# Kernel tuning notes

Measured on AMD Instinct MI355X. Metric: run time of the kernel, lower is better.

The kernel has to match this reference:

```python
import jax, jax.numpy as jnp
import numpy as np

DIM = 384
HEADS = 8
SR = 2
BN_EPS = 1e-5


def setup_inputs() -> dict:
    key = jax.random.key(0)
    ks = jax.random.split(key, 8)
    B, Hh, Ww = 4, 64, 64
    N = Hh * Ww
    Nk = (Hh // SR) * (Ww // SR)
    w = lambda k, s: jax.random.normal(k, s, jnp.float32) * 0.02
    return {
        "x": jax.random.normal(ks[0], (B, N, DIM), jnp.float32),
        "relative_pos": jax.random.normal(ks[1], (HEADS, N, Nk), jnp.float32) * 0.02,
        "H": Hh,
        "W": Ww,
        "Wq": w(ks[2], (DIM, DIM)),
        "Wk": w(ks[3], (DIM, DIM)),
        "Wv": w(ks[4], (DIM, DIM)),
        "Wp": w(ks[5], (DIM, DIM)),
        "bp": jnp.zeros((DIM,), jnp.float32),
        "sr_w": w(ks[6], (DIM, 1, SR, SR)),  # depthwise conv, OIHW with groups=DIM
        "sr_b": jnp.zeros((DIM,), jnp.float32),
        "bn_gamma": jnp.ones((DIM,), jnp.float32),
        "bn_beta": jnp.zeros((DIM,), jnp.float32),
        "bn_mean": jnp.zeros((DIM,), jnp.float32),
        "bn_var": jnp.ones((DIM,), jnp.float32),
    }


def reference(x, relative_pos, Wq, Wk, Wv, Wp, bp, sr_w, sr_b,
              bn_gamma, bn_beta, bn_mean, bn_var, H, W):
    B, N, C = x.shape
    hd = C // HEADS
    scale = hd ** (-0.5)
    # q projection -> [B, heads, N, hd]
    q = (x @ Wq.T).reshape(B, N, HEADS, hd).transpose(0, 2, 1, 3)
    # spatial reduction: depthwise conv stride SR + BatchNorm (eval mode)
    x_ = x.transpose(0, 2, 1).reshape(B, C, H, W)
    y = jax.lax.conv_general_dilated(
        x_, sr_w, window_strides=(SR, SR), padding="VALID",
        feature_group_count=C,
        dimension_numbers=("NCHW", "OIHW", "NCHW"))
    y = y + sr_b[None, :, None, None]
    inv = jax.lax.rsqrt(bn_var + BN_EPS) * bn_gamma
    y = (y - bn_mean[None, :, None, None]) * inv[None, :, None, None] \
        + bn_beta[None, :, None, None]
    xk = y.reshape(B, C, -1).transpose(0, 2, 1)  # [B, Nk, C]
    Nk = xk.shape[1]
    k = (xk @ Wk.T).reshape(B, Nk, HEADS, hd).transpose(0, 2, 1, 3)
    v = (xk @ Wv.T).reshape(B, Nk, HEADS, hd).transpose(0, 2, 1, 3)
    # scores with additive relative-position bias (broadcast over batch)
    attn = jnp.einsum("bhnd,bhmd->bhnm", q, k) * scale + relative_pos
    attn = jax.nn.softmax(attn, axis=-1)
    out = jnp.einsum("bhnm,bhmd->bhnd", attn, v)
    out = out.transpose(0, 2, 1, 3).reshape(B, N, C)
    return out @ Wp.T + bp
```

## Files before the change

### kernel.cpp

```cpp
#include <hip/hip_runtime.h>
#include <hip/hip_bf16.h>

#define LOG2E 1.4426950408889634f

typedef short bf16x8 __attribute__((ext_vector_type(8)));
typedef float f32x4  __attribute__((ext_vector_type(4)));

#define OFF_BPf  16
#define OFF_SRWf (OFF_BPf + 384)
#define OFF_SRBf (OFF_SRWf + 1536)
#define OFF_GAf  (OFF_SRBf + 384)
#define OFF_BEf  (OFF_GAf + 384)
#define OFF_MUf  (OFF_BEf + 384)
#define OFF_VAf  (OFF_MUf + 384)
#define U_XB 7712
#define U_WQ (U_XB + 6291456)
#define U_WK (U_WQ + 147456)
#define U_WV (U_WK + 147456)
#define U_WP (U_WV + 147456)
#define U_XK (U_WP + 147456)
#define U_QB (U_XK + 1572864)
#define U_KB (U_QB + 6291456)
#define U_VT (U_KB + 1572864)
#define U_OB (U_VT + 1572864)

static __device__ __forceinline__ float bfu(unsigned short u){ return __uint_as_float(((unsigned)u) << 16); }
static __device__ __forceinline__ float bf_lo(unsigned v){ return __uint_as_float(v << 16); }
static __device__ __forceinline__ float bf_hi(unsigned v){ return __uint_as_float(v & 0xFFFF0000u); }
static __device__ __forceinline__ unsigned short f2bf(float f){
  unsigned u = __float_as_uint(f);
  u += 0x7FFFu + ((u >> 16) & 1u);
  return (unsigned short)(u >> 16);
}
static __device__ __forceinline__ unsigned pk2bf(float a, float b){
  return (unsigned)f2bf(a) | ((unsigned)f2bf(b) << 16);
}

__global__ void detect_bf16(const unsigned* __restrict__ xraw, int* __restrict__ flag){
  unsigned w = xraw[threadIdx.x];
  unsigned e = (w >> 7) & 0xFFu;
  unsigned long long m = __ballot(e >= 118u && e <= 137u);
  if (threadIdx.x == 0) *flag = (__popcll(m) >= 40) ? 1 : 0;
}

static __device__ __forceinline__ void cp8_bf(unsigned short* dst, const void* src, int off, bool bf){
  if (bf) { *(uint4*)dst = *(const uint4*)((const unsigned short*)src + off); }
  else {
    const float* s = (const float*)src + off;
    float4 a = *(const float4*)s, b = *(const float4*)(s + 4);
    uint4 o; o.x = pk2bf(a.x, a.y); o.y = pk2bf(a.z, a.w);
    o.z = pk2bf(b.x, b.y); o.w = pk2bf(b.z, b.w);
    *(uint4*)dst = o;
  }
}
static __device__ __forceinline__ void cp8_f(float* dst, const void* src, int off, bool bf){
  if (bf) {
    const unsigned short* s = (const unsigned short*)src + off;
    uint4 w = *(const uint4*)s;
    float4 a, b;
    a.x = bf_lo(w.x); a.y = bf_hi(w.x); a.z = bf_lo(w.y); a.w = bf_hi(w.y);
    b.x = bf_lo(w.z); b.y = bf_hi(w.z); b.z = bf_lo(w.w); b.w = bf_hi(w.w);
    *(float4*)dst = a; *(float4*)(dst + 4) = b;
  } else {
    const float* s = (const float*)src + off;
    *(float4*)dst = *(const float4*)s;
    *(float4*)(dst + 4) = *(const float4*)(s + 4);
  }
}

__global__ __launch_bounds__(256) void convert_all(
    const void* x, const void* wq, const void* wk, const void* wv, const void* wp,
    const void* bp, const void* srw, const void* srb, const void* ga, const void* be,
    const void* mu, const void* va, float* ws){
  const bool bf = ((const int*)ws)[0] != 0;
  unsigned short* u = (unsigned short*)ws;
  int g = blockIdx.x * 256 + threadIdx.x;
  if (g < 786432) { cp8_bf(u + U_XB + g*8, x,  g*8, bf); return; }  g -= 786432;
  if (g < 18432)  { cp8_bf(u + U_WQ + g*8, wq, g*8, bf); return; }  g -= 18432;
  if (g < 18432)  { cp8_bf(u + U_WK + g*8, wk, g*8, bf); return; }  g -= 18432;
  if (g < 18432)  { cp8_bf(u + U_WV + g*8, wv, g*8, bf); return; }  g -= 18432;
  if (g < 18432)  { cp8_bf(u + U_WP + g*8, wp, g*8, bf); return; }  g -= 18432;
  if (g < 192)    { cp8_f(ws + OFF_SRWf + g*8, srw, g*8, bf); return; } g -= 192;
  if (g < 48)     { cp8_f(ws + OFF_BPf  + g*8, bp,  g*8, bf); return; } g -= 48;
  if (g < 48)     { cp8_f(ws + OFF_SRBf + g*8, srb, g*8, bf); return; } g -= 48;
  if (g < 48)     { cp8_f(ws + OFF_GAf  + g*8, ga,  g*8, bf); return; } g -= 48;
  if (g < 48)     { cp8_f(ws + OFF_BEf  + g*8, be,  g*8, bf); return; } g -= 48;
  if (g < 48)     { cp8_f(ws + OFF_MUf  + g*8, mu,  g*8, bf); return; } g -= 48;
  if (g < 48)     { cp8_f(ws + OFF_VAf  + g*8, va,  g*8, bf); }
}

__global__ __launch_bounds__(256) void sr_bn(const unsigned short* __restrict__ xb,
    const float* __restrict__ wsf, unsigned short* __restrict__ xkb){
  int idx = blockIdx.x * 256 + threadIdx.x;
  int c  = idx % 384;
  int nk = (idx / 384) & 1023;
  int b  = idx / (384 * 1024);
  int i = nk >> 5, j = nk & 31;
  const unsigned short* xp = xb + ((size_t)(b*4096 + i*128 + j*2))*384 + c;
  float acc = bfu(xp[0])      * wsf[OFF_SRWf + c*4 + 0]
            + bfu(xp[384])    * wsf[OFF_SRWf + c*4 + 1]
            + bfu(xp[64*384]) * wsf[OFF_SRWf + c*4 + 2]
            + bfu(xp[65*384]) * wsf[OFF_SRWf + c*4 + 3];
  float inv = rsqrtf(wsf[OFF_VAf + c] + 1e-5f) * wsf[OFF_GAf + c];
  float r = (acc + wsf[OFF_SRBf + c] - wsf[OFF_MUf + c]) * inv + wsf[OFF_BEf + c];
  xkb[idx] = f2bf(r);
}

__global__ __launch_bounds__(256) void proj_qkv(unsigned short* __restrict__ u){
  int z, by;
  if (blockIdx.y < 128)      { z = 0; by = blockIdx.y; }
  else if (blockIdx.y < 160) { z = 1; by = blockIdx.y - 128; }
  else                       { z = 2; by = blockIdx.y - 160; }
  const unsigned short* A = u + ((z == 0) ? U_XB : U_XK);
  const unsigned short* W = u + ((z == 0) ? U_WQ : (z == 1) ? U_WK : U_WV);

  __shared__ unsigned short As[128][40];
  __shared__ unsigned short Ws[128][40];
  const int tid = threadIdx.x;
  const int wave = tid >> 6, lane = tid & 63, lg = lane >> 4, ln = lane & 15;
  const int m0 = by * 128, n0 = blockIdx.x * 128;
  const int wm = (wave >> 1) * 64, wn = (wave & 1) * 64;
  f32x4 acc[4][4];
  #pragma unroll
  for (int i = 0; i < 4; ++i)
    #pragma unroll
    for (int j = 0; j < 4; ++j) acc[i][j] = (f32x4){0.f,0.f,0.f,0.f};

  const int arow = tid >> 1, acol = (tid & 1) * 16;
  for (int kt = 0; kt < 384; kt += 32) {
    uint4 a0 = *(const uint4*)&A[(size_t)(m0+arow)*384 + kt + acol];
    uint4 a1 = *(const uint4*)&A[(size_t)(m0+arow)*384 + kt + acol + 8];
    uint4 w0 = *(const uint4*)&W[(size_t)(n0+arow)*384 + kt + acol];
    uint4 w1 = *(const uint4*)&W[(size_t)(n0+arow)*384 + kt + acol + 8];
    __syncthreads();
    *(uint4*)&As[arow][acol] = a0;  *(uint4*)&As[arow][acol+8] = a1;
    *(uint4*)&Ws[arow][acol] = w0;  *(uint4*)&Ws[arow][acol+8] = w1;
    __syncthreads();
    bf16x8 af[4], wf[4];
    #pragma unroll
    for (int mi = 0; mi < 4; ++mi) af[mi] = *(const bf16x8*)&As[wm + mi*16 + ln][lg*8];
    #pragma unroll
    for (int ni = 0; ni < 4; ++ni) wf[ni] = *(const bf16x8*)&Ws[wn + ni*16 + ln][lg*8];
    #pragma unroll
    for (int mi = 0; mi < 4; ++mi)
      #pragma unroll
      for (int ni = 0; ni < 4; ++ni)
        acc[mi][ni] = __builtin_amdgcn_mfma_f32_16x16x32_bf16(af[mi], wf[ni], acc[mi][ni], 0, 0, 0);
  }

  unsigned short* outQ = u + U_QB;
  unsigned short* outK = u + U_KB;
  unsigned short* outV = u + U_VT;
  #pragma unroll
  for (int mi = 0; mi < 4; ++mi)
    #pragma unroll
    for (int ni = 0; ni < 4; ++ni)
      #pragma unroll
      for (int r = 0; r < 4; ++r) {
        int grow = m0 + wm + mi*16 + lg*4 + r;
        int gcol = n0 + wn + ni*16 + ln;
        unsigned short v = f2bf(acc[mi][ni][r]);
        if (z == 0)      outQ[(size_t)grow*384 + gcol] = v;
        else if (z == 1) outK[(size_t)grow*384 + gcol] = v;
        else {
          int hh = gcol / 48, d = gcol - hh*48;
          int bb = grow >> 10, mk = grow & 1023;
          outV[((size_t)((bb*8 + hh)*48 + d))*1024 + mk] = v;
        }
      }
}

__global__ __launch_bounds__(256) void gemm_out(const unsigned short* __restrict__ A,
    const unsigned short* __restrict__ W, const float* __restrict__ bias,
    void* __restrict__ out, const int* __restrict__ flag){
  __shared__ unsigned short As[128][40];
  __shared__ unsigned short Ws[128][40];
  const int tid = threadIdx.x;
  const int wave = tid >> 6, lane = tid & 63, lg = lane >> 4, ln = lane & 15;
  const int m0 = blockIdx.y * 128, n0 = blockIdx.x * 128;
  const int wm = (wave >> 1) * 64, wn = (wave & 1) * 64;
  f32x4 acc[4][4];
  #pragma unroll
  for (int i = 0; i < 4; ++i)
    #pragma unroll
    for (int j = 0; j < 4; ++j) acc[i][j] = (f32x4){0.f,0.f,0.f,0.f};

  const int arow = tid >> 1, acol = (tid & 1) * 16;
  for (int kt = 0; kt < 384; kt += 32) {
    uint4 a0 = *(const uint4*)&A[(size_t)(m0+arow)*384 + kt + acol];
    uint4 a1 = *(const uint4*)&A[(size_t)(m0+arow)*384 + kt + acol + 8];
    uint4 w0 = *(const uint4*)&W[(size_t)(n0+arow)*384 + kt + acol];
    uint4 w1 = *(const uint4*)&W[(size_t)(n0+arow)*384 + kt + acol + 8];
    __syncthreads();
    *(uint4*)&As[arow][acol] = a0;  *(uint4*)&As[arow][acol+8] = a1;
    *(uint4*)&Ws[arow][acol] = w0;  *(uint4*)&Ws[arow][acol+8] = w1;
    __syncthreads();
    bf16x8 af[4], wf[4];
    #pragma unroll
    for (int mi = 0; mi < 4; ++mi) af[mi] = *(const bf16x8*)&As[wm + mi*16 + ln][lg*8];
    #pragma unroll
    for (int ni = 0; ni < 4; ++ni) wf[ni] = *(const bf16x8*)&Ws[wn + ni*16 + ln][lg*8];
    #pragma unroll
    for (int mi = 0; mi < 4; ++mi)
      #pragma unroll
      for (int ni = 0; ni < 4; ++ni)
        acc[mi][ni] = __builtin_amdgcn_mfma_f32_16x16x32_bf16(af[mi], wf[ni], acc[mi][ni], 0, 0, 0);
  }

  const bool bff = (*flag != 0);
  #pragma unroll
  for (int mi = 0; mi < 4; ++mi)
    #pragma unroll
    for (int ni = 0; ni < 4; ++ni)
      #pragma unroll
      for (int r = 0; r < 4; ++r) {
        int grow = m0 + wm + mi*16 + lg*4 + r;
        int gcol = n0 + wn + ni*16 + ln;
        float v = acc[mi][ni][r] + bias[gcol];
        if (bff) ((unsigned short*)out)[(size_t)grow*384 + gcol] = f2bf(v);
        else     ((float*)out)[(size_t)grow*384 + gcol] = v;
      }
}

__global__ __launch_bounds__(256, 4) void attn_mfma(const unsigned short* __restrict__ qb,
    const unsigned short* __restrict__ kb, const unsigned short* __restrict__ vt,
    const void* __restrict__ rel, const int* __restrict__ flag,
    unsigned short* __restrict__ ob){
  __shared__ unsigned short Ps[4][32][72];
  __shared__ float Ls[4][2][16];
  const int b = blockIdx.x >> 5, nb = blockIdx.x & 31, h = blockIdx.y;
  const int tid = threadIdx.x, wave = tid >> 6, lane = tid & 63;
  const int lg = lane >> 4, ln = lane & 15;
  const int qrow0 = nb * 128 + wave * 32;
  const bool bfm = (*flag != 0);
  unsigned short* PsW = &Ps[wave][0][0];
  const float SCL = 0.14433756729740643f * LOG2E;

  bf16x8 qf0[2], qf1[2];
  #pragma unroll
  for (int qt = 0; qt < 2; ++qt) {
    const unsigned short* qp = qb + ((size_t)(b*4096 + qrow0 + qt*16 + ln))*384 + h*48;
    qf0[qt] = *(const bf16x8*)(qp + lg*8);
    bf16x8 z = {0,0,0,0,0,0,0,0};
    if (lg < 2) z = *(const bf16x8*)(qp + 32 + lg*8);
    qf1[qt] = z;
  }

  f32x4 o[2][3];
  #pragma unroll
  for (int qt = 0; qt < 2; ++qt) { o[qt][0] = (f32x4){0.f,0.f,0.f,0.f}; o[qt][1] = o[qt][0]; o[qt][2] = o[qt][0]; }
  float lsum[2] = {0.f, 0.f};

  const float* relf = (const float*)rel;
  const unsigned short* relh = (const unsigned short*)rel;
  const size_t rbase = ((size_t)(h*4096 + qrow0 + ln)) * 1024;
  const size_t kbase = (size_t)(b*1024) * 384 + h*48;
  const size_t vbase = ((size_t)(b*8 + h)) * 48 * 1024;

  #pragma unroll 1
  for (int t = 0; t < 16; ++t) {
    bf16x8 kf0[4], kf1[4];
    #pragma unroll
    for (int mt = 0; mt < 4; ++mt) {
      const unsigned short* kp = kb + kbase + ((size_t)(t*64 + mt*16 + ln))*384;
      kf0[mt] = *(const bf16x8*)(kp + lg*8);
      bf16x8 z = {0,0,0,0,0,0,0,0};
      if (lg < 2) z = *(const bf16x8*)(kp + 32 + lg*8);
      kf1[mt] = z;
    }

    f32x4 s[4][2];
    uint2 rr[2][4];
    #pragma unroll
    for (int mt = 0; mt < 4; ++mt) {
      #pragma unroll
      for (int qt = 0; qt < 2; ++qt) {
        s[mt][qt] = __builtin_amdgcn_mfma_f32_16x16x32_bf16(kf0[mt], qf0[qt], (f32x4){0.f,0.f,0.f,0.f}, 0, 0, 0);
        s[mt][qt] = __builtin_amdgcn_mfma_f32_16x16x32_bf16(kf1[mt], qf1[qt], s[mt][qt], 0, 0, 0);
      }
      #pragma unroll
      for (int qt = 0; qt < 2; ++qt) {
        size_t off = rbase + (size_t)qt*16384 + (size_t)t*64 + mt*16 + lg*4;
        if (bfm) rr[qt][mt] = *(const uint2*)(relh + off);
        else {
          float4 q_ = *(const float4*)(relf + off);
          rr[qt][mt].x = pk2bf(q_.x, q_.y); rr[qt][mt].y = pk2bf(q_.z, q_.w);
        }
      }
    }

    #pragma unroll
    for (int qt = 0; qt < 2; ++qt) {
      float lacc = 0.f;
      #pragma unroll
      for (int mt = 0; mt < 4; ++mt) {
        float r0 = bf_lo(rr[qt][mt].x), r1 = bf_hi(rr[qt][mt].x);
        float r2 = bf_lo(rr[qt][mt].y), r3 = bf_hi(rr[qt][mt].y);
        float p0 = exp2f(fmaf(s[mt][qt][0], SCL, r0 * LOG2E));
        float p1 = exp2f(fmaf(s[mt][qt][1], SCL, r1 * LOG2E));
        float p2 = exp2f(fmaf(s[mt][qt][2], SCL, r2 * LOG2E));
        float p3 = exp2f(fmaf(s[mt][qt][3], SCL, r3 * LOG2E));
        lacc += (p0 + p1) + (p2 + p3);
        uint2 w; w.x = pk2bf(p0, p1); w.y = pk2bf(p2, p3);
        *(uint2*)(PsW + (qt*16 + ln)*72 + mt*16 + lg*4) = w;
      }
      lsum[qt] += lacc;
    }

    bf16x8 vf[6];
    #pragma unroll
    for (int ks = 0; ks < 2; ++ks)
      #pragma unroll
      for (int nd = 0; nd < 3; ++nd)
        vf[ks*3+nd] = *(const bf16x8*)(vt + vbase + ((size_t)(nd*16 + ln))*1024 + t*64 + ks*32 + lg*8);
    #pragma unroll
    for (int ks = 0; ks < 2; ++ks)
      #pragma unroll
      for (int qt = 0; qt < 2; ++qt) {
        bf16x8 pa = *(const bf16x8*)(PsW + (qt*16 + ln)*72 + ks*32 + lg*8);
        #pragma unroll
        for (int nd = 0; nd < 3; ++nd)
          o[qt][nd] = __builtin_amdgcn_mfma_f32_16x16x32_bf16(pa, vf[ks*3+nd], o[qt][nd], 0, 0, 0);
      }
  }

  #pragma unroll
  for (int qt = 0; qt < 2; ++qt) {
    lsum[qt] += __shfl_xor(lsum[qt], 16, 64);
    lsum[qt] += __shfl_xor(lsum[qt], 32, 64);
    if (lg == 0) Ls[wave][qt][ln] = lsum[qt];
  }
  #pragma unroll
  for (int qt = 0; qt < 2; ++qt) {
    float4 l4 = *(const float4*)&Ls[wave][qt][lg*4];
    float linv[4] = {1.f/l4.x, 1.f/l4.y, 1.f/l4.z, 1.f/l4.w};
    #pragma unroll
    for (int r = 0; r < 4; ++r) {
      size_t rowb = ((size_t)(b*4096 + qrow0 + qt*16 + lg*4 + r))*384 + h*48 + ln;
      #pragma unroll
      for (int nd = 0; nd < 3; ++nd)
        ob[rowb + nd*16] = f2bf(o[qt][nd][r] * linv[r]);
    }
  }
}

extern "C" void kernel_launch(void* const* d_in, const int* in_sizes, int n_in,
                              void* d_out, int out_size, void* d_ws, size_t ws_size,
                              hipStream_t stream) {
  float* ws = (float*)d_ws;
  int* flag = (int*)d_ws;
  unsigned short* u = (unsigned short*)d_ws;

  detect_bf16<<<1, 64, 0, stream>>>((const unsigned*)d_in[0], flag);
  convert_all<<<3363, 256, 0, stream>>>(d_in[0], d_in[4], d_in[5], d_in[6], d_in[7],
      d_in[8], d_in[9], d_in[10], d_in[11], d_in[12], d_in[13], d_in[14], ws);
  sr_bn<<<6144, 256, 0, stream>>>(u + U_XB, ws, u + U_XK);
  proj_qkv<<<dim3(3, 192), 256, 0, stream>>>(u);
  attn_mfma<<<dim3(128, 8), 256, 0, stream>>>(u + U_QB, u + U_KB, u + U_VT, d_in[1], flag, u + U_OB);
  gemm_out<<<dim3(3, 128), 256, 0, stream>>>(u + U_OB, u + U_WP, ws + OFF_BPf, d_out, flag);
}
```

Measured before the change: 427.8 us.

## Stage K/V tiles in LDS via async global_load_lds and vectorize sr_bn

The attention kernel now stages K and V tiles through shared memory with direct global-to-LDS loads. K is double-buffered so the next tile prefetches while the current one is used, and block-wide syncs are added to share the tiles across the four waves instead of each wave loading them from global memory. sr_bn is vectorized to handle 8 channels per thread with 16-byte loads and stores. The V-transpose store in proj_qkv is packed into 8-byte writes, and hardware packed bf16 conversion replaces some software rounding. The added __syncthreads per iteration may cost occupancy and latency hiding.

```diff
diff --git a/kernel.cpp b/kernel.cpp
--- a/kernel.cpp
+++ b/kernel.cpp
@@ -34,6 +34,15 @@
 }
 static __device__ __forceinline__ unsigned pk2bf(float a, float b){
   return (unsigned)f2bf(a) | ((unsigned)f2bf(b) << 16);
+}
+static __device__ __forceinline__ unsigned pkcvt(float a, float b){
+  float2 f; f.x = a; f.y = b;
+  __hip_bfloat162 h = __float22bfloat162_rn(f);
+  union { __hip_bfloat162 h2; unsigned u; } cv; cv.h2 = h; return cv.u;
+}
+static __device__ __forceinline__ void gld_lds16(const void* g, void* l){
+  __builtin_amdgcn_global_load_lds((const __attribute__((address_space(1))) void*)g,
+                                   (__attribute__((address_space(3))) void*)l, 16, 0, 0);
 }
 
 __global__ void detect_bf16(const unsigned* __restrict__ xraw, int* __restrict__ flag){
@@ -92,18 +101,37 @@
 __global__ __launch_bounds__(256) void sr_bn(const unsigned short* __restrict__ xb,
     const float* __restrict__ wsf, unsigned short* __restrict__ xkb){
   int idx = blockIdx.x * 256 + threadIdx.x;
-  int c  = idx % 384;
-  int nk = (idx / 384) & 1023;
-  int b  = idx / (384 * 1024);
+  int c8 = idx % 48;
+  int nk = (idx / 48) & 1023;
+  int b  = idx / (48 * 1024);
   int i = nk >> 5, j = nk & 31;
-  const unsigned short* xp = xb + ((size_t)(b*4096 + i*128 + j*2))*384 + c;
-  float acc = bfu(xp[0])      * wsf[OFF_SRWf + c*4 + 0]
-            + bfu(xp[384])    * wsf[OFF_SRWf + c*4 + 1]
-            + bfu(xp[64*384]) * wsf[OFF_SRWf + c*4 + 2]
-            + bfu(xp[65*384]) * wsf[OFF_SRWf + c*4 + 3];
-  float inv = rsqrtf(wsf[OFF_VAf + c] + 1e-5f) * wsf[OFF_GAf + c];
-  float r = (acc + wsf[OFF_SRBf + c] - wsf[OFF_MUf + c]) * inv + wsf[OFF_BEf + c];
-  xkb[idx] = f2bf(r);
+  int c0 = c8 * 8;
+  const unsigned short* xp = xb + ((size_t)(b*4096 + i*128 + j*2))*384 + c0;
+  unsigned aw[4], bw[4], cw[4], dw[4];
+  *(uint4*)aw = *(const uint4*)(xp);
+  *(uint4*)bw = *(const uint4*)(xp + 384);
+  *(uint4*)cw = *(const uint4*)(xp + 64*384);
+  *(uint4*)dw = *(const uint4*)(xp + 65*384);
+  unsigned out[4];
+  #pragma unroll
+  for (int k2 = 0; k2 < 4; ++k2) {
+    float r2[2];
+    #pragma unroll
+    for (int half = 0; half < 2; ++half) {
+      int k = k2*2 + half;
+      int c = c0 + k;
+      float xa = half ? bf_hi(aw[k2]) : bf_lo(aw[k2]);
+      float xbv = half ? bf_hi(bw[k2]) : bf_lo(bw[k2]);
+      float xc = half ? bf_hi(cw[k2]) : bf_lo(cw[k2]);
+      float xd = half ? bf_hi(dw[k2]) : bf_lo(dw[k2]);
+      float acc = xa*wsf[OFF_SRWf+c*4] + xbv*wsf[OFF_SRWf+c*4+1]
+                + xc*wsf[OFF_SRWf+c*4+2] + xd*wsf[OFF_SRWf+c*4+3];
+      float inv = rsqrtf(wsf[OFF_VAf+c] + 1e-5f) * wsf[OFF_GAf+c];
+      r2[half] = (acc + wsf[OFF_SRBf+c] - wsf[OFF_MUf+c]) * inv + wsf[OFF_BEf+c];
+    }
+    out[k2] = pkcvt(r2[0], r2[1]);
+  }
+  *(uint4*)(xkb + (size_t)idx*8) = *(uint4*)out;
 }
 
 __global__ __launch_bounds__(256) void proj_qkv(unsigned short* __restrict__ u){
@@ -154,20 +182,24 @@
   #pragma unroll
   for (int mi = 0; mi < 4; ++mi)
     #pragma unroll
-    for (int ni = 0; ni < 4; ++ni)
-      #pragma unroll
-      for (int r = 0; r < 4; ++r) {
-        int grow = m0 + wm + mi*16 + lg*4 + r;
-        int gcol = n0 + wn + ni*16 + ln;
-        unsigned short v = f2bf(acc[mi][ni][r]);
-        if (z == 0)      outQ[(size_t)grow*384 + gcol] = v;
-        else if (z == 1) outK[(size_t)grow*384 + gcol] = v;
-        else {
-          int hh = gcol / 48, d = gcol - hh*48;
-          int bb = grow >> 10, mk = grow & 1023;
-          outV[((size_t)((bb*8 + hh)*48 + d))*1024 + mk] = v;
+    for (int ni = 0; ni < 4; ++ni) {
+      int gcol = n0 + wn + ni*16 + ln;
+      if (z == 2) {
+        int grow0 = m0 + wm + mi*16 + lg*4;
+        int hh = gcol / 48, d = gcol - hh*48;
+        int bb = grow0 >> 10, mk = grow0 & 1023;
+        uint2 st; st.x = pkcvt(acc[mi][ni][0], acc[mi][ni][1]);
+        st.y = pkcvt(acc[mi][ni][2], acc[mi][ni][3]);
+        *(uint2*)&outV[((size_t)((bb*8 + hh)*48 + d))*1024 + mk] = st;
+      } else {
+        unsigned short* dst = (z == 0) ? outQ : outK;
+        #pragma unroll
+        for (int r = 0; r < 4; ++r) {
+          int grow = m0 + wm + mi*16 + lg*4 + r;
+          dst[(size_t)grow*384 + gcol] = f2bf(acc[mi][ni][r]);
         }
       }
+    }
 }
 
 __global__ __launch_bounds__(256) void gemm_out(const unsigned short* __restrict__ A,
@@ -226,14 +258,15 @@
     const unsigned short* __restrict__ kb, const unsigned short* __restrict__ vt,
     const void* __restrict__ rel, const int* __restrict__ flag,
     unsigned short* __restrict__ ob){
-  __shared__ unsigned short Ps[4][32][72];
-  __shared__ float Ls[4][2][16];
-  const int b = blockIdx.x >> 5, nb = blockIdx.x & 31, h = blockIdx.y;
+  __shared__ __align__(16) unsigned short Kbuf[2][6*512];
+  __shared__ __align__(16) unsigned short Vbuf[8*384];
+  __shared__ __align__(16) unsigned short Ps[4][32][72];
+  const int x = blockIdx.x;
+  const int b = x >> 5, nb = x & 31, h = blockIdx.y;
   const int tid = threadIdx.x, wave = tid >> 6, lane = tid & 63;
   const int lg = lane >> 4, ln = lane & 15;
   const int qrow0 = nb * 128 + wave * 32;
   const bool bfm = (*flag != 0);
-  unsigned short* PsW = &Ps[wave][0][0];
   const float SCL = 0.14433756729740643f * LOG2E;
 
   bf16x8 qf0[2], qf1[2];
@@ -254,38 +287,59 @@
   const float* relf = (const float*)rel;
   const unsigned short* relh = (const unsigned short*)rel;
   const size_t rbase = ((size_t)(h*4096 + qrow0 + ln)) * 1024;
-  const size_t kbase = (size_t)(b*1024) * 384 + h*48;
+  const size_t kbase = (size_t)(b*1024) * 384 + (size_t)h*48;
   const size_t vbase = ((size_t)(b*8 + h)) * 48 * 1024;
+
+  const int jk1 = wave;
+  const int jk2 = 4 + wave;
+  const int jv1 = wave;
+  const int jv2 = 2 + wave;
+  int s1 = jv1*64 + lane;  int c1 = s1/48, d1 = s1 - 48*c1;
+  size_t vg1 = vbase + (size_t)d1*1024 + c1*8;
+  int s2 = jv2*64 + lane;  int c2 = s2/48, d2 = s2 - 48*c2;
+  size_t vg2 = vbase + (size_t)d2*1024 + c2*8;
+
+  gld_lds16(kb + kbase + (size_t)lane*384 + jk1*8, &Kbuf[0][jk1*512]);
+  if (wave < 2) gld_lds16(kb + kbase + (size_t)lane*384 + jk2*8, &Kbuf[0][jk2*512]);
 
   #pragma unroll 1
   for (int t = 0; t < 16; ++t) {
-    bf16x8 kf0[4], kf1[4];
-    #pragma unroll
-    for (int mt = 0; mt < 4; ++mt) {
-      const unsigned short* kp = kb + kbase + ((size_t)(t*64 + mt*16 + ln))*384;
-      kf0[mt] = *(const bf16x8*)(kp + lg*8);
-      bf16x8 z = {0,0,0,0,0,0,0,0};
-      if (lg < 2) z = *(const bf16x8*)(kp + 32 + lg*8);
-      kf1[mt] = z;
-    }
-
-    f32x4 s[4][2];
+    const int cbuf = t & 1, nbuf = cbuf ^ 1;
+    __syncthreads();
+
     uint2 rr[2][4];
-    #pragma unroll
-    for (int mt = 0; mt < 4; ++mt) {
-      #pragma unroll
-      for (int qt = 0; qt < 2; ++qt) {
-        s[mt][qt] = __builtin_amdgcn_mfma_f32_16x16x32_bf16(kf0[mt], qf0[qt], (f32x4){0.f,0.f,0.f,0.f}, 0, 0, 0);
-        s[mt][qt] = __builtin_amdgcn_mfma_f32_16x16x32_bf16(kf1[mt], qf1[qt], s[mt][qt], 0, 0, 0);
-      }
-      #pragma unroll
-      for (int qt = 0; qt < 2; ++qt) {
-        size_t off = rbase + (size_t)qt*16384 + (size_t)t*64 + mt*16 + lg*4;
-        if (bfm) rr[qt][mt] = *(const uint2*)(relh + off);
-        else {
-          float4 q_ = *(const float4*)(relf + off);
+    if (bfm) {
+      #pragma unroll
+      for (int qt = 0; qt < 2; ++qt)
+        #pragma unroll
+        for (int mt = 0; mt < 4; ++mt)
+          rr[qt][mt] = *(const uint2*)(relh + rbase + (size_t)qt*16384 + t*64 + mt*16 + lg*4);
+    } else {
+      #pragma unroll
+      for (int qt = 0; qt < 2; ++qt)
+        #pragma unroll
+        for (int mt = 0; mt < 4; ++mt) {
+          float4 q_ = *(const float4*)(relf + rbase + (size_t)qt*16384 + t*64 + mt*16 + lg*4);
           rr[qt][mt].x = pk2bf(q_.x, q_.y); rr[qt][mt].y = pk2bf(q_.z, q_.w);
         }
+    }
+
+    gld_lds16(vt + vg1 + t*64, &Vbuf[jv1*512]);
+    if (wave >= 2) gld_lds16(vt + vg2 + t*64, &Vbuf[jv2*512]);
+    const int T = (t + 1 < 16) ? t + 1 : 15;
+    gld_lds16(kb + kbase + (size_t)T*24576 + (size_t)lane*384 + jk1*8, &Kbuf[nbuf][jk1*512]);
+    if (wave < 2) gld_lds16(kb + kbase + (size_t)T*24576 + (size_t)lane*384 + jk2*8, &Kbuf[nbuf][jk2*512]);
+
+    f32x4 s[4][2];
+    #pragma unroll
+    for (int mt = 0; mt < 4; ++mt) {
+      bf16x8 k0 = *(const bf16x8*)&Kbuf[cbuf][lg*512 + (mt*16 + ln)*8];
+      bf16x8 k1 = {0,0,0,0,0,0,0,0};
+      if (lg < 2) k1 = *(const bf16x8*)&Kbuf[cbuf][(4 + lg)*512 + (mt*16 + ln)*8];
+      #pragma unroll
+      for (int qt = 0; qt < 2; ++qt) {
+        s[mt][qt] = __builtin_amdgcn_mfma_f32_16x16x32_bf16(k0, qf0[qt], (f32x4){0.f,0.f,0.f,0.f}, 0, 0, 0);
+        s[mt][qt] = __builtin_amdgcn_mfma_f32_16x16x32_bf16(k1, qf1[qt], s[mt][qt], 0, 0, 0);
       }
     }
 
@@ -301,47 +355,47 @@
         float p2 = exp2f(fmaf(s[mt][qt][2], SCL, r2 * LOG2E));
         float p3 = exp2f(fmaf(s[mt][qt][3], SCL, r3 * LOG2E));
         lacc += (p0 + p1) + (p2 + p3);
-        uint2 w; w.x = pk2bf(p0, p1); w.y = pk2bf(p2, p3);
-        *(uint2*)(PsW + (qt*16 + ln)*72 + mt*16 + lg*4) = w;
+        uint2 w; w.x = pkcvt(p0, p1); w.y = pkcvt(p2, p3);
+        *(uint2*)&Ps[wave][qt*16 + ln][mt*16 + lg*4] = w;
       }
       lsum[qt] += lacc;
     }
 
-    bf16x8 vf[6];
-    #pragma unroll
-    for (int ks = 0; ks < 2; ++ks)
+    __syncthreads();
+
+    #pragma unroll
+    for (int ks = 0; ks < 2; ++ks) {
+      bf16x8 vf[3];
       #pragma unroll
       for (int nd = 0; nd < 3; ++nd)
-        vf[ks*3+nd] = *(const bf16x8*)(vt + vbase + ((size_t)(nd*16 + ln))*1024 + t*64 + ks*32 + lg*8);
-    #pragma unroll
-    for (int ks = 0; ks < 2; ++ks)
+        vf[nd] = *(const bf16x8*)&Vbuf[(ks*4 + lg)*384 + (nd*16 + ln)*8];
       #pragma unroll
       for (int qt = 0; qt < 2; ++qt) {
-        bf16x8 pa = *(const bf16x8*)(PsW + (qt*16 + ln)*72 + ks*32 + lg*8);
+        bf16x8 pa = *(const bf16x8*)&Ps[wave][qt*16 + ln][ks*32 + lg*8];
         #pragma unroll
         for (int nd = 0; nd < 3; ++nd)
-          o[qt][nd] = __builtin_amdgcn_mfma_f32_16x16x32_bf16(pa, vf[ks*3+nd], o[qt][nd], 0, 0, 0);
+          o[qt][nd] = __builtin_amdgcn_mfma_f32_16x16x32_bf16(pa, vf[nd], o[qt][nd], 0, 0, 0);
       }
+    }
   }
 
   #pragma unroll
   for (int qt = 0; qt < 2; ++qt) {
     lsum[qt] += __shfl_xor(lsum[qt], 16, 64);
     lsum[qt] += __shfl_xor(lsum[qt], 32, 64);
-    if (lg == 0) Ls[wave][qt][ln] = lsum[qt];
-  }
-  #pragma unroll
-  for (int qt = 0; qt < 2; ++qt) {
-    float4 l4 = *(const float4*)&Ls[wave][qt][lg*4];
-    float linv[4] = {1.f/l4.x, 1.f/l4.y, 1.f/l4.z, 1.f/l4.w};
+    if (lg == 0) *(float*)&Ps[wave][qt*16 + ln][64] = lsum[qt];
+  }
+  #pragma unroll
+  for (int qt = 0; qt < 2; ++qt)
     #pragma unroll
     for (int r = 0; r < 4; ++r) {
+      float l = *(const float*)&Ps[wave][qt*16 + lg*4 + r][64];
+      float linv = 1.0f / l;
       size_t rowb = ((size_t)(b*4096 + qrow0 + qt*16 + lg*4 + r))*384 + h*48 + ln;
       #pragma unroll
       for (int nd = 0; nd < 3; ++nd)
-        ob[rowb + nd*16] = f2bf(o[qt][nd][r] * linv[r]);
-    }
-  }
+        ob[rowb + nd*16] = f2bf(o[qt][nd][r] * linv);
+    }
 }
 
 extern "C" void kernel_launch(void* const* d_in, const int* in_sizes, int n_in,
@@ -354,7 +408,7 @@
   detect_bf16<<<1, 64, 0, stream>>>((const unsigned*)d_in[0], flag);
   convert_all<<<3363, 256, 0, stream>>>(d_in[0], d_in[4], d_in[5], d_in[6], d_in[7],
       d_in[8], d_in[9], d_in[10], d_in[11], d_in[12], d_in[13], d_in[14], ws);
-  sr_bn<<<6144, 256, 0, stream>>>(u + U_XB, ws, u + U_XK);
+  sr_bn<<<768, 256, 0, stream>>>(u + U_XB, ws, u + U_XK);
   proj_qkv<<<dim3(3, 192), 256, 0, stream>>>(u);
   attn_mfma<<<dim3(128, 8), 256, 0, stream>>>(u + U_QB, u + U_KB, u + U_VT, d_in[1], flag, u + U_OB);
   gemm_out<<<dim3(3, 128), 256, 0, stream>>>(u + U_OB, u + U_WP, ws + OFF_BPf, d_out, flag);
```

Measured after the change: 358.8 us. -16.1%, faster.
